# Performance work log

Measured on AMD Instinct MI355X. Metric: run time of the kernel, lower is better.

## Reference

```python
import jax, jax.numpy as jnp
import numpy as np

K = 3  # kernel_size

def setup_inputs() -> dict:
    key = jax.random.key(0)
    k1, k2, k3 = jax.random.split(key, 3)
    B, T, G, F, O = 4, 512, 129, 96, 96
    x = jax.random.normal(k1, (B, T, G, F), dtype=jnp.float32)
    # kaiming_uniform_(a=sqrt(5)) -> bound = sqrt(6/((1+5)*fan_in)) = 1/sqrt(fan_in), fan_in = F*K
    fan_in = F * K
    wb = 1.0 / np.sqrt(fan_in)
    weight = jax.random.uniform(k2, (G, O, F, K), dtype=jnp.float32, minval=-wb, maxval=wb)
    bias = jax.random.uniform(k3, (G, O), dtype=jnp.float32, minval=-wb, maxval=wb)
    return {"x": x, "weight": weight, "bias": bias}

def reference(x, weight, bias):
    # x: [B, T, G, F]; weight: [G, O, F, K]; bias: [G, O]
    B, T, G, F = x.shape
    pad = K // 2
    xp = jnp.pad(x, ((0, 0), (pad, pad), (0, 0), (0, 0)))  # [B, T+2p, G, F]
    # gather K shifted views -> [B, T, G, F, K] (same windows as unfold with padding K//2)
    xw = jnp.stack([xp[:, k:k + T] for k in range(K)], axis=-1)
    out = jnp.einsum('btgfk,gofk->btgo', xw, weight)
    out = out + bias  # broadcast [G, O] over [B, T, G, O]
    return out
```

## Files before the change

### kernel.cpp

```cpp
#include <hip/hip_runtime.h>
#include <hip/hip_bf16.h>

typedef unsigned short ushort_t;
typedef __attribute__((ext_vector_type(8))) short short8;
typedef __attribute__((ext_vector_type(4))) float floatx4;

#define G_  129
#define F_  96
#define O_  96
#define T_  512
#define KD  288
#define LDA 40
#define LDB 296

__device__ __forceinline__ ushort_t f2bf(float f) {
    unsigned u = __builtin_bit_cast(unsigned, f);
    u += 0x7FFFu + ((u >> 16) & 1u);
    return (ushort_t)(u >> 16);
}

__global__ void wt_permute(const float* __restrict__ w, ushort_t* __restrict__ wt) {
    int i = blockIdx.x * 256 + threadIdx.x;
    const int total = G_ * O_ * KD;
    if (i >= total) return;
    int base = i / KD;
    int kd = i - base * KD;
    int kk = kd / F_;
    int f  = kd - kk * F_;
    wt[i] = f2bf(w[base * KD + f * 3 + kk]);
}

__global__ __launch_bounds__(256, 2) void conv_mfma(
    const float* __restrict__ x, const ushort_t* __restrict__ wt,
    const float* __restrict__ bias, float* __restrict__ out)
{
    __shared__ __align__(16) ushort_t Wl[O_ * LDB];
    __shared__ __align__(16) ushort_t Xl[2][128 * LDA];

    const int g   = blockIdx.y;
    const int m0  = blockIdx.x * 128;
    const int tid = threadIdx.x;
    const int wave = tid >> 6;
    const int lane = tid & 63;
    const int ln = lane & 15;
    const int q  = lane >> 4;

    {
        const ushort_t* src = wt + (size_t)g * (O_ * KD);
        for (int idx = tid; idx < O_ * 36; idx += 256) {
            int o = idx / 36;
            int s = idx - o * 36;
            *(short8*)&Wl[o * LDB + s * 8] = *(const short8*)&src[o * KD + s * 8];
        }
    }

    auto stageA = [&](int c) {
        int kk = c / 3;
        int fb = (c - kk * 3) * 32;
        int buf = c & 1;
        #pragma unroll
        for (int i = 0; i < 2; ++i) {
            int idx = tid + i * 256;
            int r = idx >> 2;
            int seg = idx & 3;
            int m = m0 + r;
            int b = m >> 9;
            int t = m & 511;
            int tt = t + kk - 1;
            short8 v = {0,0,0,0,0,0,0,0};
            if ((unsigned)tt < (unsigned)T_) {
                const float* p = x + ((size_t)((b * T_ + tt) * G_ + g) * F_ + fb + seg * 8);
                floatx4 f0 = *(const floatx4*)p;
                floatx4 f1 = *(const floatx4*)(p + 4);
                v[0] = (short)f2bf(f0[0]); v[1] = (short)f2bf(f0[1]);
                v[2] = (short)f2bf(f0[2]); v[3] = (short)f2bf(f0[3]);
                v[4] = (short)f2bf(f1[0]); v[5] = (short)f2bf(f1[1]);
                v[6] = (short)f2bf(f1[2]); v[7] = (short)f2bf(f1[3]);
            }
            *(short8*)&Xl[buf][r * LDA + seg * 8] = v;
        }
    };

    floatx4 acc[2][6];
    #pragma unroll
    for (int s = 0; s < 2; ++s)
        #pragma unroll
        for (int nt = 0; nt < 6; ++nt)
            acc[s][nt] = (floatx4){0.f, 0.f, 0.f, 0.f};

    stageA(0);
    __syncthreads();

    for (int c = 0; c < 9; ++c) {
        if (c < 8) stageA(c + 1);
        int buf = c & 1;
        const short8 a0 = *(const short8*)&Xl[buf][(wave * 32 + ln) * LDA + q * 8];
        const short8 a1 = *(const short8*)&Xl[buf][(wave * 32 + 16 + ln) * LDA + q * 8];
        #pragma unroll
        for (int nt = 0; nt < 6; ++nt) {
            const short8 bb = *(const short8*)&Wl[(nt * 16 + ln) * LDB + c * 32 + q * 8];
            acc[0][nt] = __builtin_amdgcn_mfma_f32_16x16x32_bf16(a0, bb, acc[0][nt], 0, 0, 0);
            acc[1][nt] = __builtin_amdgcn_mfma_f32_16x16x32_bf16(a1, bb, acc[1][nt], 0, 0, 0);
        }
        __syncthreads();
    }

    #pragma unroll
    for (int s = 0; s < 2; ++s) {
        int mbase = m0 + wave * 32 + s * 16 + q * 4;
        #pragma unroll
        for (int nt = 0; nt < 6; ++nt) {
            int o = nt * 16 + ln;
            float bv = bias[g * O_ + o];
            #pragma unroll
            for (int r = 0; r < 4; ++r) {
                int m = mbase + r;
                out[(size_t)(m * G_ + g) * O_ + o] = acc[s][nt][r] + bv;
            }
        }
    }
}

extern "C" void kernel_launch(void* const* d_in, const int* in_sizes, int n_in,
                              void* d_out, int out_size, void* d_ws, size_t ws_size,
                              hipStream_t stream) {
    const float* x    = (const float*)d_in[0];
    const float* w    = (const float*)d_in[1];
    const float* bias = (const float*)d_in[2];
    float* out = (float*)d_out;
    ushort_t* wt = (ushort_t*)d_ws;

    const int total_w = G_ * O_ * KD;
    wt_permute<<<dim3((total_w + 255) / 256), dim3(256), 0, stream>>>(w, wt);

    dim3 grid(2048 / 128, G_);
    conv_mfma<<<grid, dim3(256), 0, stream>>>(x, wt, bias, out);
}
```

Baseline: 244.9 us.

## Load activation fragments directly into registers, drop LDS staging and barriers

Replaces the double-buffered LDS staging of the input tile with per-lane direct global loads of the exact MFMA A-fragment, register-prefetched one chunk ahead, so the per-chunk __syncthreads goes away. The block grows to 512 threads covering 256 rows, which halves how often each block reloads the weight slice into LDS. In exchange the global loads are 32-byte strided per lane rather than coalesced staging, and register pressure rises under launch bounds of 4 blocks per SM.

```diff
diff --git a/kernel.cpp b/kernel.cpp
--- a/kernel.cpp
+++ b/kernel.cpp
@@ -10,7 +10,6 @@
 #define O_  96
 #define T_  512
 #define KD  288
-#define LDA 40
 #define LDB 296
 
 __device__ __forceinline__ ushort_t f2bf(float f) {
@@ -30,56 +29,34 @@
     wt[i] = f2bf(w[base * KD + f * 3 + kk]);
 }
 
-__global__ __launch_bounds__(256, 2) void conv_mfma(
+__global__ __launch_bounds__(512, 4) void conv_mfma(
     const float* __restrict__ x, const ushort_t* __restrict__ wt,
     const float* __restrict__ bias, float* __restrict__ out)
 {
     __shared__ __align__(16) ushort_t Wl[O_ * LDB];
-    __shared__ __align__(16) ushort_t Xl[2][128 * LDA];
 
-    const int g   = blockIdx.y;
-    const int m0  = blockIdx.x * 128;
-    const int tid = threadIdx.x;
+    const int g    = blockIdx.y;
+    const int m0   = blockIdx.x * 256;
+    const int tid  = threadIdx.x;
     const int wave = tid >> 6;
     const int lane = tid & 63;
-    const int ln = lane & 15;
-    const int q  = lane >> 4;
+    const int ln   = lane & 15;
+    const int q    = lane >> 4;
 
     {
         const ushort_t* src = wt + (size_t)g * (O_ * KD);
-        for (int idx = tid; idx < O_ * 36; idx += 256) {
+        for (int idx = tid; idx < O_ * 36; idx += 512) {
             int o = idx / 36;
             int s = idx - o * 36;
             *(short8*)&Wl[o * LDB + s * 8] = *(const short8*)&src[o * KD + s * 8];
         }
     }
+    __syncthreads();
 
-    auto stageA = [&](int c) {
-        int kk = c / 3;
-        int fb = (c - kk * 3) * 32;
-        int buf = c & 1;
-        #pragma unroll
-        for (int i = 0; i < 2; ++i) {
-            int idx = tid + i * 256;
-            int r = idx >> 2;
-            int seg = idx & 3;
-            int m = m0 + r;
-            int b = m >> 9;
-            int t = m & 511;
-            int tt = t + kk - 1;
-            short8 v = {0,0,0,0,0,0,0,0};
-            if ((unsigned)tt < (unsigned)T_) {
-                const float* p = x + ((size_t)((b * T_ + tt) * G_ + g) * F_ + fb + seg * 8);
-                floatx4 f0 = *(const floatx4*)p;
-                floatx4 f1 = *(const floatx4*)(p + 4);
-                v[0] = (short)f2bf(f0[0]); v[1] = (short)f2bf(f0[1]);
-                v[2] = (short)f2bf(f0[2]); v[3] = (short)f2bf(f0[3]);
-                v[4] = (short)f2bf(f1[0]); v[5] = (short)f2bf(f1[1]);
-                v[6] = (short)f2bf(f1[2]); v[7] = (short)f2bf(f1[3]);
-            }
-            *(short8*)&Xl[buf][r * LDA + seg * 8] = v;
-        }
-    };
+    const int r0 = m0 + wave * 32 + ln;
+    const int r1 = r0 + 16;
+    const int b0 = r0 >> 9, t0 = r0 & 511;
+    const int b1 = r1 >> 9, t1 = r1 & 511;
 
     floatx4 acc[2][6];
     #pragma unroll
@@ -88,21 +65,51 @@
         for (int nt = 0; nt < 6; ++nt)
             acc[s][nt] = (floatx4){0.f, 0.f, 0.f, 0.f};
 
-    stageA(0);
-    __syncthreads();
+    auto issue = [&](int c, floatx4* f, bool* vld) {
+        int kk = c / 3;
+        int fb = (c - kk * 3) * 32;
+        int tt0 = t0 + kk - 1, tt1 = t1 + kk - 1;
+        vld[0] = (unsigned)tt0 < (unsigned)T_;
+        vld[1] = (unsigned)tt1 < (unsigned)T_;
+        int tc0 = tt0 < 0 ? 0 : (tt0 > T_ - 1 ? T_ - 1 : tt0);
+        int tc1 = tt1 < 0 ? 0 : (tt1 > T_ - 1 ? T_ - 1 : tt1);
+        const float* p0 = x + ((size_t)((b0 * T_ + tc0) * G_ + g) * F_ + fb + q * 8);
+        const float* p1 = x + ((size_t)((b1 * T_ + tc1) * G_ + g) * F_ + fb + q * 8);
+        f[0] = *(const floatx4*)p0;
+        f[1] = *(const floatx4*)(p0 + 4);
+        f[2] = *(const floatx4*)p1;
+        f[3] = *(const floatx4*)(p1 + 4);
+    };
 
+    floatx4 pf[4];
+    bool pv[2];
+    issue(0, pf, pv);
+
+    #pragma unroll
     for (int c = 0; c < 9; ++c) {
-        if (c < 8) stageA(c + 1);
-        int buf = c & 1;
-        const short8 a0 = *(const short8*)&Xl[buf][(wave * 32 + ln) * LDA + q * 8];
-        const short8 a1 = *(const short8*)&Xl[buf][(wave * 32 + 16 + ln) * LDA + q * 8];
+        floatx4 cur0 = pf[0], cur1 = pf[1], cur2 = pf[2], cur3 = pf[3];
+        bool cv0 = pv[0], cv1 = pv[1];
+        if (c < 8) issue(c + 1, pf, pv);
+
+        short8 a0, a1;
+        a0[0] = (short)f2bf(cur0[0]); a0[1] = (short)f2bf(cur0[1]);
+        a0[2] = (short)f2bf(cur0[2]); a0[3] = (short)f2bf(cur0[3]);
+        a0[4] = (short)f2bf(cur1[0]); a0[5] = (short)f2bf(cur1[1]);
+        a0[6] = (short)f2bf(cur1[2]); a0[7] = (short)f2bf(cur1[3]);
+        a1[0] = (short)f2bf(cur2[0]); a1[1] = (short)f2bf(cur2[1]);
+        a1[2] = (short)f2bf(cur2[2]); a1[3] = (short)f2bf(cur2[3]);
+        a1[4] = (short)f2bf(cur3[0]); a1[5] = (short)f2bf(cur3[1]);
+        a1[6] = (short)f2bf(cur3[2]); a1[7] = (short)f2bf(cur3[3]);
+        const short8 z = {0, 0, 0, 0, 0, 0, 0, 0};
+        if (!cv0) a0 = z;
+        if (!cv1) a1 = z;
+
         #pragma unroll
         for (int nt = 0; nt < 6; ++nt) {
             const short8 bb = *(const short8*)&Wl[(nt * 16 + ln) * LDB + c * 32 + q * 8];
             acc[0][nt] = __builtin_amdgcn_mfma_f32_16x16x32_bf16(a0, bb, acc[0][nt], 0, 0, 0);
             acc[1][nt] = __builtin_amdgcn_mfma_f32_16x16x32_bf16(a1, bb, acc[1][nt], 0, 0, 0);
         }
-        __syncthreads();
     }
 
     #pragma unroll
@@ -133,6 +140,6 @@
     const int total_w = G_ * O_ * KD;
     wt_permute<<<dim3((total_w + 255) / 256), dim3(256), 0, stream>>>(w, wt);
 
-    dim3 grid(2048 / 128, G_);
-    conv_mfma<<<grid, dim3(256), 0, stream>>>(x, wt, bias, out);
+    dim3 grid(2048 / 256, G_);
+    conv_mfma<<<grid, dim3(512), 0, stream>>>(x, wt, bias, out);
 }
```

After: 239.2 us. 2.4% less time.
